# Kernel optimization log

Hardware: AMD Instinct MI355X
Metric: run time of the kernel (lower is better)

The kernel has to match this reference:

```python
import jax, jax.numpy as jnp
import numpy as np

EPS = 1e-6

def layer_norm_2d(x, w, b):
    # channel-first LayerNorm over dim 1 of (B, C, H, W)
    u = x.mean(axis=1, keepdims=True)
    s = ((x - u) ** 2).mean(axis=1, keepdims=True)
    xn = (x - u) / jnp.sqrt(s + EPS)
    return w[None, :, None, None] * xn + b[None, :, None, None]


def setup_inputs() -> dict:
    key = jax.random.key(0)
    ks = jax.random.split(key, 5)
    B, C, H, W = 2, 256, 48, 48
    mem_dim, T = 64, 5
    x = jax.random.normal(ks[0], (B, C, H, W), jnp.float32)
    keys = jax.random.normal(ks[1], (B, mem_dim, T, H, W), jnp.float32)
    vals = jax.random.normal(ks[2], (B, mem_dim, T, H, W), jnp.float32)
    wq = jax.random.normal(ks[3], (mem_dim, C), jnp.float32) * 0.05
    wo = jax.random.normal(ks[4], (C, mem_dim), jnp.float32) * 0.05
    wg = jax.random.normal(jax.random.fold_in(key, 7), (C, 2 * C), jnp.float32) * 0.05
    return {
        "x": x, "keys": keys, "vals": vals,
        "wq": wq, "lnq_w": jnp.ones((mem_dim,), jnp.float32), "lnq_b": jnp.zeros((mem_dim,), jnp.float32),
        "wo": wo, "lno_w": jnp.ones((C,), jnp.float32), "lno_b": jnp.zeros((C,), jnp.float32),
        "wg": wg, "bg": jnp.zeros((C,), jnp.float32),
    }


def reference(x, keys, vals, wq, lnq_w, lnq_b, wo, lno_w, lno_b, wg, bg):
    B, C, H, W = x.shape
    mem_dim = wq.shape[0]
    nh = 4
    hd = mem_dim // nh
    scale = hd ** -0.5

    # query projection: 1x1 conv + LayerNorm2d
    q = jnp.einsum('oc,bchw->bohw', wq, x)            # (B, mem_dim, H, W)
    q = layer_norm_2d(q, lnq_w, lnq_b)
    q = q.reshape(B, mem_dim, H * W).transpose(0, 2, 1)      # (B, HW, mem_dim)
    q = q.reshape(B, H * W, nh, hd).transpose(0, 2, 1, 3)    # (B, nh, HW, hd)

    # memory bank: (B, mem_dim, T, Hm, Wm) -> (B, nh, L, hd)
    _, _, T, Hm, Wm = keys.shape
    L = T * Hm * Wm
    k = keys.transpose(0, 2, 3, 4, 1).reshape(B, L, nh, hd).transpose(0, 2, 1, 3)
    v = vals.transpose(0, 2, 3, 4, 1).reshape(B, L, nh, hd).transpose(0, 2, 1, 3)

    attn = jnp.einsum('bnqd,bnkd->bnqk', q, k) * scale       # (B, nh, HW, L)
    attn = jax.nn.softmax(attn, axis=-1)
    mem = jnp.einsum('bnqk,bnkd->bnqd', attn, v)             # (B, nh, HW, hd)
    mem = mem.transpose(0, 2, 1, 3).reshape(B, H * W, mem_dim)
    mem = mem.transpose(0, 2, 1).reshape(B, mem_dim, H, W)

    # output projection: 1x1 conv + LayerNorm2d
    mem_out = jnp.einsum('om,bmhw->bohw', wo, mem)
    mem_out = layer_norm_2d(mem_out, lno_w, lno_b)

    # sigmoid-gated residual fusion
    cat = jnp.concatenate([x, mem_out], axis=1)              # (B, 2C, H, W)
    gate = jax.nn.sigmoid(jnp.einsum('oc,bchw->bohw', wg, cat) + bg[None, :, None, None])
    return x + gate * mem_out
```

## Files before the change

kernel.cpp:

```cpp
#include <hip/hip_runtime.h>
#include <hip/hip_bf16.h>

#define B_   2
#define C_   256
#define HW_  2304
#define MD_  64
#define NH_  4
#define HD_  16
#define LL_  11520
#define EPS_ 1e-6f
#define NUMSZ (B_ * HW_ * MD_)
#define DENSZ (B_ * HW_ * 4)

typedef __attribute__((ext_vector_type(8)))  short    short8;
typedef __attribute__((ext_vector_type(16))) float    f32x16;
typedef __attribute__((ext_vector_type(4)))  unsigned u32x4;

__device__ __forceinline__ unsigned pk2(float a, float b) {
  unsigned short lo = __builtin_bit_cast(unsigned short, __float2bfloat16(a));
  unsigned short hi = __builtin_bit_cast(unsigned short, __float2bfloat16(b));
  return (unsigned)lo | ((unsigned)hi << 16);
}

__global__ __launch_bounds__(256) void kT(const float* __restrict__ keys,
                                          const float* __restrict__ vals,
                                          __hip_bfloat16* __restrict__ kt,
                                          __hip_bfloat16* __restrict__ vt)
{
  __shared__ float tile[16][256];
  const int bn = blockIdx.x / 45;
  const int l0 = (blockIdx.x % 45) * 256;
  const int tid = threadIdx.x;
  const float* kbase = keys + (size_t)bn * 16 * LL_ + l0;
  const float* vbase = vals + (size_t)bn * 16 * LL_ + l0;
  __hip_bfloat16* vout = vt + (size_t)bn * 18 * LL_ + l0;
  #pragma unroll
  for (int d = 0; d < 16; ++d) {
    tile[d][tid] = kbase[d * LL_ + tid];
    vout[d * LL_ + tid] = __float2bfloat16(vbase[d * LL_ + tid]);
  }
  vout[16 * LL_ + tid] = __float2bfloat16(1.0f);
  vout[17 * LL_ + tid] = __float2bfloat16(0.0f);
  __syncthreads();
  __hip_bfloat16* ko = kt + ((size_t)bn * LL_ + l0 + tid) * 16;
  u32x4 w0, w1;
  #pragma unroll
  for (int j = 0; j < 4; ++j) w0[j] = pk2(tile[2*j][tid],   tile[2*j+1][tid]);
  #pragma unroll
  for (int j = 0; j < 4; ++j) w1[j] = pk2(tile[8+2*j][tid], tile[8+2*j+1][tid]);
  ((u32x4*)ko)[0] = w0;
  ((u32x4*)ko)[1] = w1;
}

__global__ __launch_bounds__(256) void kW(const float* __restrict__ wo,
                                          const float* __restrict__ wg,
                                          const float* __restrict__ wq,
                                          __hip_bfloat16* __restrict__ wop,
                                          __hip_bfloat16* __restrict__ wgp,
                                          __hip_bfloat16* __restrict__ wqp)
{
  const int tid = threadIdx.x;
  const int unit = blockIdx.x * 4 + (tid >> 6);
  const int l = tid & 63;
  u32x4 wv;
  if (unit < 256) {
    const int t = unit >> 5, ks = unit & 31;
    const float* src = wg + (size_t)(t * 32 + (l & 31)) * 512 + ks * 16 + (l >> 5) * 8;
    #pragma unroll
    for (int j = 0; j < 4; ++j) wv[j] = pk2(src[2*j], src[2*j+1]);
    *(u32x4*)(wgp + ((size_t)unit * 64 + l) * 8) = wv;
  } else if (unit < 288) {
    const int v = unit - 256;
    const int t = v >> 2, ks = v & 3;
    const float* src = wo + (size_t)(t * 32 + (l & 31)) * 64 + ks * 16 + (l >> 5) * 8;
    #pragma unroll
    for (int j = 0; j < 4; ++j) wv[j] = pk2(src[2*j], src[2*j+1]);
    *(u32x4*)(wop + ((size_t)v * 64 + l) * 8) = wv;
  } else {
    const int v = unit - 288;
    const int t = v >> 4, ks = v & 15;
    const float* src = wq + (size_t)(t * 32 + (l & 31)) * 256 + ks * 16 + (l >> 5) * 8;
    #pragma unroll
    for (int j = 0; j < 4; ++j) wv[j] = pk2(src[2*j], src[2*j+1]);
    *(u32x4*)(wqp + ((size_t)v * 64 + l) * 8) = wv;
  }
}

__global__ __launch_bounds__(128) void kA(const float* __restrict__ x,
                                          const __hip_bfloat16* __restrict__ wqp,
                                          const float* __restrict__ lnw,
                                          const float* __restrict__ lnb,
                                          __hip_bfloat16* __restrict__ qb)
{
  __shared__ __align__(16) unsigned char xl[16384];
  __shared__ float red_s[2][32], red_q[2][32];
  __shared__ float lnwl[64], lnbl[64];

  const int tid = threadIdx.x;
  const int pix0 = blockIdx.x * 32;
  const int b = pix0 / HW_, sp0 = pix0 % HW_;

  if (tid < 64) { lnwl[tid] = lnw[tid]; lnbl[tid] = lnb[tid]; }

  #pragma unroll 8
  for (int it = 0; it < 32; ++it) {
    const int u = tid + it * 128;
    const int pix = u & 31, cp = u >> 5;
    const float a0 = x[((size_t)(b * C_ + 2 * cp)) * HW_ + sp0 + pix];
    const float a1 = x[((size_t)(b * C_ + 2 * cp + 1)) * HW_ + sp0 + pix];
    *(unsigned*)(xl + pix * 512 + ((4 * cp) ^ ((pix & 7) << 4))) = pk2(a0, a1);
  }
  __syncthreads();

  const int w = tid >> 6, l = tid & 63, col = l & 31, hi = l >> 5;
  const int swz = (col & 7) << 4;

  f32x16 acc;
  #pragma unroll
  for (int i = 0; i < 16; ++i) acc[i] = 0.f;
  #pragma unroll
  for (int ks = 0; ks < 16; ++ks) {
    const u32x4 af = *(const u32x4*)(wqp + ((size_t)((w * 16 + ks) * 64 + l)) * 8);
    const u32x4 bf = *(const u32x4*)(xl + col * 512 + (((ks * 16 + hi * 8) * 2) ^ swz));
    acc = __builtin_amdgcn_mfma_f32_32x32x16_bf16(
        __builtin_bit_cast(short8, af), __builtin_bit_cast(short8, bf), acc, 0, 0, 0);
  }

  float s = 0.f, q = 0.f;
  #pragma unroll
  for (int r = 0; r < 16; ++r) { s += acc[r]; q += acc[r] * acc[r]; }
  s += __shfl_xor(s, 32);
  q += __shfl_xor(q, 32);
  if (hi == 0) { red_s[w][col] = s; red_q[w][col] = q; }
  __syncthreads();
  const float su = red_s[0][col] + red_s[1][col];
  const float qu = red_q[0][col] + red_q[1][col];
  const float u_  = su * (1.f / 64.f);
  const float var = qu * (1.f / 64.f) - u_ * u_;
  const float inv = rsqrtf(var + EPS_);
  const float QS  = 0.25f * 1.4426950408889634f;

  #pragma unroll
  for (int r = 0; r < 16; r += 2) {
    const int ch = w * 32 + (r & 3) + 8 * (r >> 2) + 4 * hi;
    const float q0v = (lnwl[ch]   * ((acc[r]   - u_) * inv) + lnbl[ch])   * QS;
    const float q1v = (lnwl[ch+1] * ((acc[r+1] - u_) * inv) + lnbl[ch+1]) * QS;
    const int n = ch >> 4, d = ch & 15;
    *(unsigned*)(qb + ((size_t)(b * NH_ + n) * HW_ + sp0 + col) * 16 + d) = pk2(q0v, q1v);
  }
}

__global__ __launch_bounds__(256) void kB(const __hip_bfloat16* __restrict__ qb,
                                          const __hip_bfloat16* __restrict__ kt,
                                          const __hip_bfloat16* __restrict__ vt,
                                          float* __restrict__ num,
                                          float* __restrict__ den)
{
  __shared__ float red[4][32][17];
  const int blk = blockIdx.x;
  const int bn = blk & 7;
  const int qt = (blk >> 3) % 72;
  const int h  = blk / 576;
  const int b = bn >> 2, n = bn & 3;
  const int tid = threadIdx.x;
  const int wv = tid >> 6;
  const int l  = tid & 63;
  const int col = l & 31;
  const int hi  = l >> 5;
  const int q0 = qt * 32;

  const u32x4 qf = *(const u32x4*)(qb + ((size_t)bn * HW_ + q0 + col) * 16 + hi * 8);
  const short8 qv = __builtin_bit_cast(short8, qf);

  const __hip_bfloat16* pK = kt + ((size_t)bn * LL_ + col) * 16 + hi * 8;
  const int d2 = (col < 17) ? col : 17;
  const __hip_bfloat16* pV = vt + ((size_t)(bn * 18 + d2)) * LL_ + hi * 8;

  f32x16 acc;
  #pragma unroll
  for (int i = 0; i < 16; ++i) acc[i] = 0.f;

  const int kbeg = (h * 4 + wv) * 1440;

  u32x4 kc = *(const u32x4*)(pK + (size_t)kbeg * 16);
  u32x4 va = *(const u32x4*)(pV + kbeg);
  u32x4 vb = *(const u32x4*)(pV + kbeg + 16);

  for (int t = 0; t < 45; ++t) {
    const int l0 = kbeg + t * 32;
    const int ln = (t < 44) ? (l0 + 32) : kbeg;
    u32x4 kn  = *(const u32x4*)(pK + (size_t)ln * 16);
    u32x4 van = *(const u32x4*)(pV + ln);
    u32x4 vbn = *(const u32x4*)(pV + ln + 16);

    f32x16 s;
    #pragma unroll
    for (int i = 0; i < 16; ++i) s[i] = 0.f;
    s = __builtin_amdgcn_mfma_f32_32x32x16_bf16(__builtin_bit_cast(short8, kc), qv, s, 0, 0, 0);

    float pt[16];
    #pragma unroll
    for (int i = 0; i < 16; ++i) pt[i] = __builtin_amdgcn_exp2f(s[i]);

    {
      unsigned p0 = pk2(pt[0], pt[1]), p1 = pk2(pt[2], pt[3]);
      unsigned p2 = pk2(pt[4], pt[5]), p3 = pk2(pt[6], pt[7]);
      asm volatile("v_permlane32_swap_b32 %0, %1" : "+v"(p0), "+v"(p2));
      asm volatile("v_permlane32_swap_b32 %0, %1" : "+v"(p1), "+v"(p3));
      u32x4 pa; pa[0] = p0; pa[1] = p1; pa[2] = p2; pa[3] = p3;
      acc = __builtin_amdgcn_mfma_f32_32x32x16_bf16(
          __builtin_bit_cast(short8, pa), __builtin_bit_cast(short8, va), acc, 0, 0, 0);
    }
    {
      unsigned p0 = pk2(pt[8],  pt[9]),  p1 = pk2(pt[10], pt[11]);
      unsigned p2 = pk2(pt[12], pt[13]), p3 = pk2(pt[14], pt[15]);
      asm volatile("v_permlane32_swap_b32 %0, %1" : "+v"(p0), "+v"(p2));
      asm volatile("v_permlane32_swap_b32 %0, %1" : "+v"(p1), "+v"(p3));
      u32x4 pa; pa[0] = p0; pa[1] = p1; pa[2] = p2; pa[3] = p3;
      acc = __builtin_amdgcn_mfma_f32_32x32x16_bf16(
          __builtin_bit_cast(short8, pa), __builtin_bit_cast(short8, vb), acc, 0, 0, 0);
    }
    kc = kn; va = van; vb = vbn;
  }

  if (col <= 16) {
    #pragma unroll
    for (int r = 0; r < 16; ++r) {
      const int row = (r & 3) + 8 * (r >> 2) + 4 * hi;
      red[wv][row][col] = acc[r];
    }
  }
  __syncthreads();
  float* numh = num + (size_t)h * NUMSZ;
  float* denh = den + (size_t)h * DENSZ;
  #pragma unroll
  for (int idx = tid; idx < 512; idx += 256) {
    const int row = idx >> 4, c = idx & 15;
    numh[((size_t)b * HW_ + q0 + row) * MD_ + n * HD_ + c] =
        red[0][row][c] + red[1][row][c] + red[2][row][c] + red[3][row][c];
  }
  if (tid < 32) {
    denh[((size_t)b * HW_ + q0 + tid) * 4 + n] =
        red[0][tid][16] + red[1][tid][16] + red[2][tid][16] + red[3][tid][16];
  }
}

__global__ __launch_bounds__(512) void kC(const float* __restrict__ x,
                                          const float* __restrict__ num,
                                          const float* __restrict__ den,
                                          const __hip_bfloat16* __restrict__ wop,
                                          const __hip_bfloat16* __restrict__ wgp,
                                          const float* __restrict__ lnw,
                                          const float* __restrict__ lnb,
                                          const float* __restrict__ bg,
                                          float* __restrict__ out)
{
  __shared__ __align__(16) unsigned char xl[16384];
  __shared__ __align__(16) unsigned char mol[16384];
  __shared__ __align__(16) unsigned char ml[4096];
  __shared__ float red_s[8][32], red_q[8][32];
  __shared__ float lnwl[256], lnbl[256], bgl[256];

  const int tid = threadIdx.x;
  const int pix0 = blockIdx.x * 32;
  const int b = pix0 / HW_, sp0 = pix0 % HW_;

  if (tid < 256) { lnwl[tid] = lnw[tid]; lnbl[tid] = lnb[tid]; bgl[tid] = bg[tid]; }

  #pragma unroll
  for (int it = 0; it < 8; ++it) {
    const int u = tid + it * 512;
    const int pix = u & 31, cp = u >> 5;
    const float a0 = x[((size_t)(b * C_ + 2 * cp)) * HW_ + sp0 + pix];
    const float a1 = x[((size_t)(b * C_ + 2 * cp + 1)) * HW_ + sp0 + pix];
    *(unsigned*)(xl + pix * 512 + ((4 * cp) ^ ((pix & 7) << 4))) = pk2(a0, a1);
  }
  #pragma unroll
  for (int it = 0; it < 2; ++it) {
    const int u = tid + it * 512;
    const int mp = u & 31, pix = u >> 5;
    const size_t base = ((size_t)(b * HW_ + sp0 + pix)) * MD_ + 2 * mp;
    const float2 a0 = *(const float2*)(num + base);
    const float2 a1 = *(const float2*)(num + NUMSZ + base);
    const size_t di = ((size_t)(b * HW_ + sp0 + pix)) * 4 + (mp >> 3);
    const float r = 1.f / (den[di] + den[DENSZ + di]);
    *(unsigned*)(ml + pix * 128 + ((4 * mp) ^ ((pix & 7) << 4))) =
        pk2((a0.x + a1.x) * r, (a0.y + a1.y) * r);
  }
  __syncthreads();

  const int w = tid >> 6, l = tid & 63, col = l & 31, hi = l >> 5;
  const int swz = (col & 7) << 4;

  f32x16 acc;
  #pragma unroll
  for (int i = 0; i < 16; ++i) acc[i] = 0.f;
  #pragma unroll
  for (int ks = 0; ks < 4; ++ks) {
    const u32x4 af = *(const u32x4*)(wop + ((size_t)((w * 4 + ks) * 64 + l)) * 8);
    const u32x4 bf = *(const u32x4*)(ml + col * 128 + (((ks * 16 + hi * 8) * 2) ^ swz));
    acc = __builtin_amdgcn_mfma_f32_32x32x16_bf16(
        __builtin_bit_cast(short8, af), __builtin_bit_cast(short8, bf), acc, 0, 0, 0);
  }

  float s = 0.f, q = 0.f;
  #pragma unroll
  for (int r = 0; r < 16; ++r) { s += acc[r]; q += acc[r] * acc[r]; }
  s += __shfl_xor(s, 32);
  q += __shfl_xor(q, 32);
  if (hi == 0) { red_s[w][col] = s; red_q[w][col] = q; }
  __syncthreads();
  float su = 0.f, qu = 0.f;
  #pragma unroll
  for (int ww = 0; ww < 8; ++ww) { su += red_s[ww][col]; qu += red_q[ww][col]; }
  const float u_  = su * (1.f / 256.f);
  const float var = qu * (1.f / 256.f) - u_ * u_;
  const float inv = rsqrtf(var + EPS_);

  float moln[16];
  #pragma unroll
  for (int r = 0; r < 16; ++r) {
    const int ch = w * 32 + (r & 3) + 8 * (r >> 2) + 4 * hi;
    moln[r] = lnwl[ch] * ((acc[r] - u_) * inv) + lnbl[ch];
  }
  #pragma unroll
  for (int r = 0; r < 16; r += 2) {
    const int ch = w * 32 + (r & 3) + 8 * (r >> 2) + 4 * hi;
    *(unsigned*)(mol + col * 512 + ((2 * ch) ^ swz)) = pk2(moln[r], moln[r + 1]);
  }
  __syncthreads();

  f32x16 acc2;
  #pragma unroll
  for (int i = 0; i < 16; ++i) acc2[i] = 0.f;
  #pragma unroll
  for (int ks = 0; ks < 16; ++ks) {
    const u32x4 af = *(const u32x4*)(wgp + ((size_t)((w * 32 + ks) * 64 + l)) * 8);
    const u32x4 bf = *(const u32x4*)(xl + col * 512 + (((ks * 16 + hi * 8) * 2) ^ swz));
    acc2 = __builtin_amdgcn_mfma_f32_32x32x16_bf16(
        __builtin_bit_cast(short8, af), __builtin_bit_cast(short8, bf), acc2, 0, 0, 0);
  }
  #pragma unroll
  for (int ks = 0; ks < 16; ++ks) {
    const u32x4 af = *(const u32x4*)(wgp + ((size_t)((w * 32 + 16 + ks) * 64 + l)) * 8);
    const u32x4 bf = *(const u32x4*)(mol + col * 512 + (((ks * 16 + hi * 8) * 2) ^ swz));
    acc2 = __builtin_amdgcn_mfma_f32_32x32x16_bf16(
        __builtin_bit_cast(short8, af), __builtin_bit_cast(short8, bf), acc2, 0, 0, 0);
  }

  #pragma unroll
  for (int r = 0; r < 16; ++r) {
    const int ch = w * 32 + (r & 3) + 8 * (r >> 2) + 4 * hi;
    const size_t idx = ((size_t)(b * C_ + ch)) * HW_ + sp0 + col;
    const float z = acc2[r] + bgl[ch];
    const float gate = 1.f / (1.f + __expf(-z));
    out[idx] = x[idx] + gate * moln[r];
  }
}

extern "C" void kernel_launch(void* const* d_in, const int* in_sizes, int n_in,
                              void* d_out, int out_size, void* d_ws, size_t ws_size,
                              hipStream_t stream)
{
  const float* x    = (const float*)d_in[0];
  const float* keys = (const float*)d_in[1];
  const float* vals = (const float*)d_in[2];
  const float* wq   = (const float*)d_in[3];
  const float* lnqw = (const float*)d_in[4];
  const float* lnqb = (const float*)d_in[5];
  const float* wo   = (const float*)d_in[6];
  const float* lnow = (const float*)d_in[7];
  const float* lnob = (const float*)d_in[8];
  const float* wg   = (const float*)d_in[9];
  const float* bg   = (const float*)d_in[10];
  float* out = (float*)d_out;

  __hip_bfloat16* qbf = (__hip_bfloat16*)d_ws;
  __hip_bfloat16* kt  = qbf + (size_t)B_ * NH_ * HW_ * HD_;
  __hip_bfloat16* vt  = kt + (size_t)B_ * NH_ * LL_ * HD_;
  __hip_bfloat16* wgp = vt + (size_t)B_ * NH_ * 18 * LL_;
  __hip_bfloat16* wop = wgp + (size_t)256 * 64 * 8;
  __hip_bfloat16* wqp = wop + (size_t)32 * 64 * 8;
  float* numws = (float*)(wqp + (size_t)32 * 64 * 8);
  float* denws = numws + 2 * (size_t)NUMSZ;

  kT<<<360, 256, 0, stream>>>(keys, vals, kt, vt);
  kW<<<80, 256, 0, stream>>>(wo, wg, wq, wop, wgp, wqp);
  kA<<<144, 128, 0, stream>>>(x, wqp, lnqw, lnqb, qbf);
  kB<<<1152, 256, 0, stream>>>(qbf, kt, vt, numws, denws);
  kC<<<144, 512, 0, stream>>>(x, numws, denws, wop, wgp, lnow, lnob, bg, out);
}
```

Measured before the change: 149.4 us.

## Merge prep kernels into one launch and software-pipeline QK MFMA in attention

Three preprocessing kernels (K/V transpose, weight packing, query projection) become one kernel, kP2, with block-index dispatch. This removes two launches and the inter-kernel gaps. The query projection now reads and converts wq to bf16 inline and handles 64 pixels per block, so the separate wq packing step goes away. The attention loop now issues the next tile's QK MFMA before the current exp/PV step and prefetches two tiles ahead to hide latency, at the cost of more registers. A dead, incomplete kP kernel is left in the file unused.

```diff
diff --git a/kernel.cpp b/kernel.cpp
--- a/kernel.cpp
+++ b/kernel.cpp
@@ -22,131 +22,212 @@
   return (unsigned)lo | ((unsigned)hi << 16);
 }
 
-__global__ __launch_bounds__(256) void kT(const float* __restrict__ keys,
+__global__ __launch_bounds__(256) void kP(const float* __restrict__ keys,
                                           const float* __restrict__ vals,
+                                          const float* __restrict__ wq,
+                                          const float* __restrict__ wo,
+                                          const float* __restrict__ wg,
+                                          const float* __restrict__ lnw,
+                                          const float* __restrict__ lnb,
                                           __hip_bfloat16* __restrict__ kt,
-                                          __hip_bfloat16* __restrict__ vt)
-{
-  __shared__ float tile[16][256];
-  const int bn = blockIdx.x / 45;
-  const int l0 = (blockIdx.x % 45) * 256;
-  const int tid = threadIdx.x;
-  const float* kbase = keys + (size_t)bn * 16 * LL_ + l0;
-  const float* vbase = vals + (size_t)bn * 16 * LL_ + l0;
-  __hip_bfloat16* vout = vt + (size_t)bn * 18 * LL_ + l0;
-  #pragma unroll
-  for (int d = 0; d < 16; ++d) {
-    tile[d][tid] = kbase[d * LL_ + tid];
-    vout[d * LL_ + tid] = __float2bfloat16(vbase[d * LL_ + tid]);
-  }
-  vout[16 * LL_ + tid] = __float2bfloat16(1.0f);
-  vout[17 * LL_ + tid] = __float2bfloat16(0.0f);
-  __syncthreads();
-  __hip_bfloat16* ko = kt + ((size_t)bn * LL_ + l0 + tid) * 16;
-  u32x4 w0, w1;
-  #pragma unroll
-  for (int j = 0; j < 4; ++j) w0[j] = pk2(tile[2*j][tid],   tile[2*j+1][tid]);
-  #pragma unroll
-  for (int j = 0; j < 4; ++j) w1[j] = pk2(tile[8+2*j][tid], tile[8+2*j+1][tid]);
-  ((u32x4*)ko)[0] = w0;
-  ((u32x4*)ko)[1] = w1;
-}
-
-__global__ __launch_bounds__(256) void kW(const float* __restrict__ wo,
-                                          const float* __restrict__ wg,
-                                          const float* __restrict__ wq,
+                                          __hip_bfloat16* __restrict__ vt,
                                           __hip_bfloat16* __restrict__ wop,
                                           __hip_bfloat16* __restrict__ wgp,
-                                          __hip_bfloat16* __restrict__ wqp)
-{
-  const int tid = threadIdx.x;
-  const int unit = blockIdx.x * 4 + (tid >> 6);
-  const int l = tid & 63;
-  u32x4 wv;
-  if (unit < 256) {
-    const int t = unit >> 5, ks = unit & 31;
-    const float* src = wg + (size_t)(t * 32 + (l & 31)) * 512 + ks * 16 + (l >> 5) * 8;
-    #pragma unroll
-    for (int j = 0; j < 4; ++j) wv[j] = pk2(src[2*j], src[2*j+1]);
-    *(u32x4*)(wgp + ((size_t)unit * 64 + l) * 8) = wv;
-  } else if (unit < 288) {
-    const int v = unit - 256;
-    const int t = v >> 2, ks = v & 3;
-    const float* src = wo + (size_t)(t * 32 + (l & 31)) * 64 + ks * 16 + (l >> 5) * 8;
-    #pragma unroll
-    for (int j = 0; j < 4; ++j) wv[j] = pk2(src[2*j], src[2*j+1]);
-    *(u32x4*)(wop + ((size_t)v * 64 + l) * 8) = wv;
-  } else {
-    const int v = unit - 288;
-    const int t = v >> 4, ks = v & 15;
-    const float* src = wq + (size_t)(t * 32 + (l & 31)) * 256 + ks * 16 + (l >> 5) * 8;
-    #pragma unroll
-    for (int j = 0; j < 4; ++j) wv[j] = pk2(src[2*j], src[2*j+1]);
-    *(u32x4*)(wqp + ((size_t)v * 64 + l) * 8) = wv;
-  }
-}
-
-__global__ __launch_bounds__(128) void kA(const float* __restrict__ x,
-                                          const __hip_bfloat16* __restrict__ wqp,
-                                          const float* __restrict__ lnw,
-                                          const float* __restrict__ lnb,
                                           __hip_bfloat16* __restrict__ qb)
 {
-  __shared__ __align__(16) unsigned char xl[16384];
-  __shared__ float red_s[2][32], red_q[2][32];
+  __shared__ __align__(16) unsigned char lds_buf[32768];
+  __shared__ float red_s[2][2][32], red_q[2][2][32];
   __shared__ float lnwl[64], lnbl[64];
 
+  const int blk = blockIdx.x;
   const int tid = threadIdx.x;
-  const int pix0 = blockIdx.x * 32;
-  const int b = pix0 / HW_, sp0 = pix0 % HW_;
-
-  if (tid < 64) { lnwl[tid] = lnw[tid]; lnbl[tid] = lnb[tid]; }
-
-  #pragma unroll 8
-  for (int it = 0; it < 32; ++it) {
-    const int u = tid + it * 128;
-    const int pix = u & 31, cp = u >> 5;
-    const float a0 = x[((size_t)(b * C_ + 2 * cp)) * HW_ + sp0 + pix];
-    const float a1 = x[((size_t)(b * C_ + 2 * cp + 1)) * HW_ + sp0 + pix];
-    *(unsigned*)(xl + pix * 512 + ((4 * cp) ^ ((pix & 7) << 4))) = pk2(a0, a1);
-  }
-  __syncthreads();
-
-  const int w = tid >> 6, l = tid & 63, col = l & 31, hi = l >> 5;
-  const int swz = (col & 7) << 4;
-
-  f32x16 acc;
-  #pragma unroll
-  for (int i = 0; i < 16; ++i) acc[i] = 0.f;
-  #pragma unroll
-  for (int ks = 0; ks < 16; ++ks) {
-    const u32x4 af = *(const u32x4*)(wqp + ((size_t)((w * 16 + ks) * 64 + l)) * 8);
-    const u32x4 bf = *(const u32x4*)(xl + col * 512 + (((ks * 16 + hi * 8) * 2) ^ swz));
-    acc = __builtin_amdgcn_mfma_f32_32x32x16_bf16(
-        __builtin_bit_cast(short8, af), __builtin_bit_cast(short8, bf), acc, 0, 0, 0);
-  }
-
-  float s = 0.f, q = 0.f;
-  #pragma unroll
-  for (int r = 0; r < 16; ++r) { s += acc[r]; q += acc[r] * acc[r]; }
-  s += __shfl_xor(s, 32);
-  q += __shfl_xor(q, 32);
-  if (hi == 0) { red_s[w][col] = s; red_q[w][col] = q; }
-  __syncthreads();
-  const float su = red_s[0][col] + red_s[1][col];
-  const float qu = red_q[0][col] + red_q[1][col];
-  const float u_  = su * (1.f / 64.f);
-  const float var = qu * (1.f / 64.f) - u_ * u_;
-  const float inv = rsqrtf(var + EPS_);
-  const float QS  = 0.25f * 1.4426950408889634f;
-
-  #pragma unroll
-  for (int r = 0; r < 16; r += 2) {
-    const int ch = w * 32 + (r & 3) + 8 * (r >> 2) + 4 * hi;
-    const float q0v = (lnwl[ch]   * ((acc[r]   - u_) * inv) + lnbl[ch])   * QS;
-    const float q1v = (lnwl[ch+1] * ((acc[r+1] - u_) * inv) + lnbl[ch+1]) * QS;
-    const int n = ch >> 4, d = ch & 15;
-    *(unsigned*)(qb + ((size_t)(b * NH_ + n) * HW_ + sp0 + col) * 16 + d) = pk2(q0v, q1v);
+
+  if (blk < 360) {
+    float* tile = (float*)lds_buf;
+    const int bn = blk / 45;
+    const int l0 = (blk % 45) * 256;
+    const float* kbase = keys + (size_t)bn * 16 * LL_ + l0;
+    const float* vbase = vals + (size_t)bn * 16 * LL_ + l0;
+    __hip_bfloat16* vout = vt + (size_t)bn * 18 * LL_ + l0;
+    #pragma unroll
+    for (int d = 0; d < 16; ++d) {
+      tile[d * 256 + tid] = kbase[d * LL_ + tid];
+      vout[d * LL_ + tid] = __float2bfloat16(vbase[d * LL_ + tid]);
+    }
+    vout[16 * LL_ + tid] = __float2bfloat16(1.0f);
+    vout[17 * LL_ + tid] = __float2bfloat16(0.0f);
+    __syncthreads();
+    __hip_bfloat16* ko = kt + ((size_t)bn * LL_ + l0 + tid) * 16;
+    u32x4 w0, w1;
+    #pragma unroll
+    for (int j = 0; j < 4; ++j) w0[j] = pk2(tile[(2*j) * 256 + tid],   tile[(2*j+1) * 256 + tid]);
+    #pragma unroll
+    for (int j = 0; j < 4; ++j) w1[j] = pk2(tile[(8+2*j) * 256 + tid], tile[(9+2*j) * 256 + tid]);
+    ((u32x4*)ko)[0] = w0;
+    ((u32x4*)ko)[1] = w1;
+  } else if (blk < 432) {
+    const int unit = (blk - 360) * 4 + (tid >> 6);
+    const int l = tid & 63;
+    u32x4 wv;
+    if (unit < 256) {
+      const int t = unit >> 5, ks = unit & 31;
+      const float* src = wg + (size_t)(t * 32 + (l & 31)) * 512 + ks * 16 + (l >> 5) * 8;
+      #pragma unroll
+      for (int j = 0; j < 4; ++j) wv[j] = pk2(src[2*j], src[2*j+1]);
+      *(u32x4*)(wgp + ((size_t)unit * 64 + l) * 8) = wv;
+    } else {
+      const int v = unit - 256;
+      const int t = v >> 2, ks = v & 3;
+      const float* src = wo + (size_t)(t * 32 + (l & 31)) * 64 + ks * 16 + (l >> 5) * 8;
+      #pragma unroll
+      for (int j = 0; j < 4; ++j) wv[j] = pk2(src[2*j], src[2*j+1]);
+      *(u32x4*)(wop + ((size_t)v * 64 + l) * 8) = wv;
+    }
+  } else {
+    const float* x = keys;
+    (void)x;
+    const int ablk = blk - 432;
+    const int pix0 = ablk * 64;
+    const int b = pix0 / HW_, sp0 = pix0 % HW_;
+    unsigned char* xl = lds_buf;
+
+    if (tid < 64) { lnwl[tid] = lnw[tid]; lnbl[tid] = lnb[tid]; }
+
+    const float* xin = lnw - 0;
+    (void)xin;
+    ;
+    const float* xp = (const float*)lnb;
+    (void)xp;
+    {
+      extern __shared__ unsigned char dummy_never[];
+      (void)dummy_never;
+    }
+  }
+}
+
+__global__ __launch_bounds__(256) void kP2(const float* __restrict__ keys,
+                                           const float* __restrict__ vals,
+                                           const float* __restrict__ x,
+                                           const float* __restrict__ wq,
+                                           const float* __restrict__ wo,
+                                           const float* __restrict__ wg,
+                                           const float* __restrict__ lnw,
+                                           const float* __restrict__ lnb,
+                                           __hip_bfloat16* __restrict__ kt,
+                                           __hip_bfloat16* __restrict__ vt,
+                                           __hip_bfloat16* __restrict__ wop,
+                                           __hip_bfloat16* __restrict__ wgp,
+                                           __hip_bfloat16* __restrict__ qb)
+{
+  __shared__ __align__(16) unsigned char lds_buf[32768];
+  __shared__ float red_s[2][2][32], red_q[2][2][32];
+  __shared__ float lnwl[64], lnbl[64];
+
+  const int blk = blockIdx.x;
+  const int tid = threadIdx.x;
+
+  if (blk < 360) {
+    float* tile = (float*)lds_buf;
+    const int bn = blk / 45;
+    const int l0 = (blk % 45) * 256;
+    const float* kbase = keys + (size_t)bn * 16 * LL_ + l0;
+    const float* vbase = vals + (size_t)bn * 16 * LL_ + l0;
+    __hip_bfloat16* vout = vt + (size_t)bn * 18 * LL_ + l0;
+    #pragma unroll
+    for (int d = 0; d < 16; ++d) {
+      tile[d * 256 + tid] = kbase[d * LL_ + tid];
+      vout[d * LL_ + tid] = __float2bfloat16(vbase[d * LL_ + tid]);
+    }
+    vout[16 * LL_ + tid] = __float2bfloat16(1.0f);
+    vout[17 * LL_ + tid] = __float2bfloat16(0.0f);
+    __syncthreads();
+    __hip_bfloat16* ko = kt + ((size_t)bn * LL_ + l0 + tid) * 16;
+    u32x4 w0, w1;
+    #pragma unroll
+    for (int j = 0; j < 4; ++j) w0[j] = pk2(tile[(2*j) * 256 + tid],   tile[(2*j+1) * 256 + tid]);
+    #pragma unroll
+    for (int j = 0; j < 4; ++j) w1[j] = pk2(tile[(8+2*j) * 256 + tid], tile[(9+2*j) * 256 + tid]);
+    ((u32x4*)ko)[0] = w0;
+    ((u32x4*)ko)[1] = w1;
+  } else if (blk < 432) {
+    const int unit = (blk - 360) * 4 + (tid >> 6);
+    const int l = tid & 63;
+    u32x4 wv;
+    if (unit < 256) {
+      const int t = unit >> 5, ks = unit & 31;
+      const float* src = wg + (size_t)(t * 32 + (l & 31)) * 512 + ks * 16 + (l >> 5) * 8;
+      #pragma unroll
+      for (int j = 0; j < 4; ++j) wv[j] = pk2(src[2*j], src[2*j+1]);
+      *(u32x4*)(wgp + ((size_t)unit * 64 + l) * 8) = wv;
+    } else {
+      const int v = unit - 256;
+      const int t = v >> 2, ks = v & 3;
+      const float* src = wo + (size_t)(t * 32 + (l & 31)) * 64 + ks * 16 + (l >> 5) * 8;
+      #pragma unroll
+      for (int j = 0; j < 4; ++j) wv[j] = pk2(src[2*j], src[2*j+1]);
+      *(u32x4*)(wop + ((size_t)v * 64 + l) * 8) = wv;
+    }
+  } else {
+    const int ablk = blk - 432;
+    const int pix0 = ablk * 64;
+    const int b = pix0 / HW_, sp0 = pix0 % HW_;
+    unsigned char* xl = lds_buf;
+
+    if (tid < 64) { lnwl[tid] = lnw[tid]; lnbl[tid] = lnb[tid]; }
+
+    #pragma unroll 8
+    for (int it = 0; it < 32; ++it) {
+      const int u = tid + it * 256;
+      const int pix = u & 63, cp = u >> 6;
+      const float a0 = x[((size_t)(b * C_ + 2 * cp)) * HW_ + sp0 + pix];
+      const float a1 = x[((size_t)(b * C_ + 2 * cp + 1)) * HW_ + sp0 + pix];
+      *(unsigned*)(xl + pix * 512 + ((4 * cp) ^ ((pix & 7) << 4))) = pk2(a0, a1);
+    }
+    __syncthreads();
+
+    const int wv4 = tid >> 6, l = tid & 63, col = l & 31, hi = l >> 5;
+    const int g = wv4 >> 1, w = wv4 & 1;
+    const int p = g * 32 + col;
+    const int swz = (p & 7) << 4;
+
+    f32x16 acc;
+    #pragma unroll
+    for (int i = 0; i < 16; ++i) acc[i] = 0.f;
+    #pragma unroll 4
+    for (int ks = 0; ks < 16; ++ks) {
+      const float* src = wq + (size_t)(w * 32 + col) * 256 + ks * 16 + hi * 8;
+      const float4 f0 = *(const float4*)src;
+      const float4 f1 = *(const float4*)(src + 4);
+      u32x4 af;
+      af[0] = pk2(f0.x, f0.y); af[1] = pk2(f0.z, f0.w);
+      af[2] = pk2(f1.x, f1.y); af[3] = pk2(f1.z, f1.w);
+      const u32x4 bf = *(const u32x4*)(xl + p * 512 + (((ks * 16 + hi * 8) * 2) ^ swz));
+      acc = __builtin_amdgcn_mfma_f32_32x32x16_bf16(
+          __builtin_bit_cast(short8, af), __builtin_bit_cast(short8, bf), acc, 0, 0, 0);
+    }
+
+    float s = 0.f, q = 0.f;
+    #pragma unroll
+    for (int r = 0; r < 16; ++r) { s += acc[r]; q += acc[r] * acc[r]; }
+    s += __shfl_xor(s, 32);
+    q += __shfl_xor(q, 32);
+    if (hi == 0) { red_s[g][w][col] = s; red_q[g][w][col] = q; }
+    __syncthreads();
+    const float su = red_s[g][0][col] + red_s[g][1][col];
+    const float qu = red_q[g][0][col] + red_q[g][1][col];
+    const float u_  = su * (1.f / 64.f);
+    const float var = qu * (1.f / 64.f) - u_ * u_;
+    const float inv = rsqrtf(var + EPS_);
+    const float QS  = 0.25f * 1.4426950408889634f;
+
+    #pragma unroll
+    for (int r = 0; r < 16; r += 2) {
+      const int ch = w * 32 + (r & 3) + 8 * (r >> 2) + 4 * hi;
+      const float q0v = (lnwl[ch]   * ((acc[r]   - u_) * inv) + lnbl[ch])   * QS;
+      const float q1v = (lnwl[ch+1] * ((acc[r+1] - u_) * inv) + lnbl[ch+1]) * QS;
+      const int n = ch >> 4, d = ch & 15;
+      *(unsigned*)(qb + ((size_t)(b * NH_ + n) * HW_ + sp0 + p) * 16 + d) = pk2(q0v, q1v);
+    }
   }
 }
 
@@ -176,31 +257,33 @@
   const int d2 = (col < 17) ? col : 17;
   const __hip_bfloat16* pV = vt + ((size_t)(bn * 18 + d2)) * LL_ + hi * 8;
 
-  f32x16 acc;
-  #pragma unroll
-  for (int i = 0; i < 16; ++i) acc[i] = 0.f;
+  f32x16 acc, zac;
+  #pragma unroll
+  for (int i = 0; i < 16; ++i) { acc[i] = 0.f; zac[i] = 0.f; }
 
   const int kbeg = (h * 4 + wv) * 1440;
 
-  u32x4 kc = *(const u32x4*)(pK + (size_t)kbeg * 16);
-  u32x4 va = *(const u32x4*)(pV + kbeg);
-  u32x4 vb = *(const u32x4*)(pV + kbeg + 16);
+  u32x4 kc0 = *(const u32x4*)(pK + (size_t)kbeg * 16);
+  u32x4 va  = *(const u32x4*)(pV + kbeg);
+  u32x4 vb  = *(const u32x4*)(pV + kbeg + 16);
+  f32x16 s_cur = __builtin_amdgcn_mfma_f32_32x32x16_bf16(
+      __builtin_bit_cast(short8, kc0), qv, zac, 0, 0, 0);
+  u32x4 kc1 = *(const u32x4*)(pK + (size_t)(kbeg + 32) * 16);
+  u32x4 va1 = *(const u32x4*)(pV + kbeg + 32);
+  u32x4 vb1 = *(const u32x4*)(pV + kbeg + 48);
 
   for (int t = 0; t < 45; ++t) {
-    const int l0 = kbeg + t * 32;
-    const int ln = (t < 44) ? (l0 + 32) : kbeg;
-    u32x4 kn  = *(const u32x4*)(pK + (size_t)ln * 16);
-    u32x4 van = *(const u32x4*)(pV + ln);
-    u32x4 vbn = *(const u32x4*)(pV + ln + 16);
-
-    f32x16 s;
-    #pragma unroll
-    for (int i = 0; i < 16; ++i) s[i] = 0.f;
-    s = __builtin_amdgcn_mfma_f32_32x32x16_bf16(__builtin_bit_cast(short8, kc), qv, s, 0, 0, 0);
-
     float pt[16];
     #pragma unroll
-    for (int i = 0; i < 16; ++i) pt[i] = __builtin_amdgcn_exp2f(s[i]);
+    for (int i = 0; i < 16; ++i) pt[i] = __builtin_amdgcn_exp2f(s_cur[i]);
+
+    f32x16 s_next = __builtin_amdgcn_mfma_f32_32x32x16_bf16(
+        __builtin_bit_cast(short8, kc1), qv, zac, 0, 0, 0);
+
+    const int l2 = (t < 43) ? (kbeg + (t + 2) * 32) : kbeg;
+    u32x4 kc2 = *(const u32x4*)(pK + (size_t)l2 * 16);
+    u32x4 va2 = *(const u32x4*)(pV + l2);
+    u32x4 vb2 = *(const u32x4*)(pV + l2 + 16);
 
     {
       unsigned p0 = pk2(pt[0], pt[1]), p1 = pk2(pt[2], pt[3]);
@@ -220,7 +303,10 @@
       acc = __builtin_amdgcn_mfma_f32_32x32x16_bf16(
           __builtin_bit_cast(short8, pa), __builtin_bit_cast(short8, vb), acc, 0, 0, 0);
     }
-    kc = kn; va = van; vb = vbn;
+
+    s_cur = s_next;
+    kc1 = kc2;
+    va = va1; vb = vb1; va1 = va2; vb1 = vb2;
   }
 
   if (col <= 16) {
@@ -380,13 +466,11 @@
   __hip_bfloat16* vt  = kt + (size_t)B_ * NH_ * LL_ * HD_;
   __hip_bfloat16* wgp = vt + (size_t)B_ * NH_ * 18 * LL_;
   __hip_bfloat16* wop = wgp + (size_t)256 * 64 * 8;
-  __hip_bfloat16* wqp = wop + (size_t)32 * 64 * 8;
-  float* numws = (float*)(wqp + (size_t)32 * 64 * 8);
+  float* numws = (float*)(wop + (size_t)32 * 64 * 8);
   float* denws = numws + 2 * (size_t)NUMSZ;
 
-  kT<<<360, 256, 0, stream>>>(keys, vals, kt, vt);
-  kW<<<80, 256, 0, stream>>>(wo, wg, wq, wop, wgp, wqp);
-  kA<<<144, 128, 0, stream>>>(x, wqp, lnqw, lnqb, qbf);
+  kP2<<<504, 256, 0, stream>>>(keys, vals, x, wq, wo, wg, lnqw, lnqb,
+                               kt, vt, wop, wgp, qbf);
   kB<<<1152, 256, 0, stream>>>(qbf, kt, vt, numws, denws);
   kC<<<144, 512, 0, stream>>>(x, numws, denws, wop, wgp, lnow, lnob, bg, out);
 }
```

After: 146.9 us. Within noise of the previous version (-1.7%).

## Merge prep kernels into one launch and split attention keys four ways

Applied to the files above, without the earlier changes.

Three preprocessing kernels (K/V transpose, weight packing, query projection) become one launch that branches on block index. The query projection now reads and converts wq from fp32 directly instead of using a prepacked copy. The attention kernel moves from 4 waves per block to 2, with the key range split into 4 chunks across 2304 blocks. The final kernel therefore sums 4 partial numerators and denominators. The aim is fewer launches and more independent blocks, at the cost of larger partial buffers and extra reduction reads.

```diff
diff --git a/kernel.cpp b/kernel.cpp
--- a/kernel.cpp
+++ b/kernel.cpp
@@ -22,141 +22,139 @@
   return (unsigned)lo | ((unsigned)hi << 16);
 }
 
-__global__ __launch_bounds__(256) void kT(const float* __restrict__ keys,
+__global__ __launch_bounds__(256) void kP(const float* __restrict__ keys,
                                           const float* __restrict__ vals,
+                                          const float* __restrict__ x,
+                                          const float* __restrict__ wq,
+                                          const float* __restrict__ wo,
+                                          const float* __restrict__ wg,
+                                          const float* __restrict__ lnw,
+                                          const float* __restrict__ lnb,
                                           __hip_bfloat16* __restrict__ kt,
-                                          __hip_bfloat16* __restrict__ vt)
-{
-  __shared__ float tile[16][256];
-  const int bn = blockIdx.x / 45;
-  const int l0 = (blockIdx.x % 45) * 256;
-  const int tid = threadIdx.x;
-  const float* kbase = keys + (size_t)bn * 16 * LL_ + l0;
-  const float* vbase = vals + (size_t)bn * 16 * LL_ + l0;
-  __hip_bfloat16* vout = vt + (size_t)bn * 18 * LL_ + l0;
-  #pragma unroll
-  for (int d = 0; d < 16; ++d) {
-    tile[d][tid] = kbase[d * LL_ + tid];
-    vout[d * LL_ + tid] = __float2bfloat16(vbase[d * LL_ + tid]);
-  }
-  vout[16 * LL_ + tid] = __float2bfloat16(1.0f);
-  vout[17 * LL_ + tid] = __float2bfloat16(0.0f);
-  __syncthreads();
-  __hip_bfloat16* ko = kt + ((size_t)bn * LL_ + l0 + tid) * 16;
-  u32x4 w0, w1;
-  #pragma unroll
-  for (int j = 0; j < 4; ++j) w0[j] = pk2(tile[2*j][tid],   tile[2*j+1][tid]);
-  #pragma unroll
-  for (int j = 0; j < 4; ++j) w1[j] = pk2(tile[8+2*j][tid], tile[8+2*j+1][tid]);
-  ((u32x4*)ko)[0] = w0;
-  ((u32x4*)ko)[1] = w1;
-}
-
-__global__ __launch_bounds__(256) void kW(const float* __restrict__ wo,
-                                          const float* __restrict__ wg,
-                                          const float* __restrict__ wq,
+                                          __hip_bfloat16* __restrict__ vt,
                                           __hip_bfloat16* __restrict__ wop,
                                           __hip_bfloat16* __restrict__ wgp,
-                                          __hip_bfloat16* __restrict__ wqp)
-{
-  const int tid = threadIdx.x;
-  const int unit = blockIdx.x * 4 + (tid >> 6);
-  const int l = tid & 63;
-  u32x4 wv;
-  if (unit < 256) {
-    const int t = unit >> 5, ks = unit & 31;
-    const float* src = wg + (size_t)(t * 32 + (l & 31)) * 512 + ks * 16 + (l >> 5) * 8;
-    #pragma unroll
-    for (int j = 0; j < 4; ++j) wv[j] = pk2(src[2*j], src[2*j+1]);
-    *(u32x4*)(wgp + ((size_t)unit * 64 + l) * 8) = wv;
-  } else if (unit < 288) {
-    const int v = unit - 256;
-    const int t = v >> 2, ks = v & 3;
-    const float* src = wo + (size_t)(t * 32 + (l & 31)) * 64 + ks * 16 + (l >> 5) * 8;
-    #pragma unroll
-    for (int j = 0; j < 4; ++j) wv[j] = pk2(src[2*j], src[2*j+1]);
-    *(u32x4*)(wop + ((size_t)v * 64 + l) * 8) = wv;
-  } else {
-    const int v = unit - 288;
-    const int t = v >> 4, ks = v & 15;
-    const float* src = wq + (size_t)(t * 32 + (l & 31)) * 256 + ks * 16 + (l >> 5) * 8;
-    #pragma unroll
-    for (int j = 0; j < 4; ++j) wv[j] = pk2(src[2*j], src[2*j+1]);
-    *(u32x4*)(wqp + ((size_t)v * 64 + l) * 8) = wv;
-  }
-}
-
-__global__ __launch_bounds__(128) void kA(const float* __restrict__ x,
-                                          const __hip_bfloat16* __restrict__ wqp,
-                                          const float* __restrict__ lnw,
-                                          const float* __restrict__ lnb,
                                           __hip_bfloat16* __restrict__ qb)
 {
-  __shared__ __align__(16) unsigned char xl[16384];
-  __shared__ float red_s[2][32], red_q[2][32];
+  __shared__ __align__(16) unsigned char lds_buf[32768];
+  __shared__ float red_s[2][2][32], red_q[2][2][32];
   __shared__ float lnwl[64], lnbl[64];
 
+  const int blk = blockIdx.x;
   const int tid = threadIdx.x;
-  const int pix0 = blockIdx.x * 32;
-  const int b = pix0 / HW_, sp0 = pix0 % HW_;
-
-  if (tid < 64) { lnwl[tid] = lnw[tid]; lnbl[tid] = lnb[tid]; }
-
-  #pragma unroll 8
-  for (int it = 0; it < 32; ++it) {
-    const int u = tid + it * 128;
-    const int pix = u & 31, cp = u >> 5;
-    const float a0 = x[((size_t)(b * C_ + 2 * cp)) * HW_ + sp0 + pix];
-    const float a1 = x[((size_t)(b * C_ + 2 * cp + 1)) * HW_ + sp0 + pix];
-    *(unsigned*)(xl + pix * 512 + ((4 * cp) ^ ((pix & 7) << 4))) = pk2(a0, a1);
-  }
-  __syncthreads();
-
-  const int w = tid >> 6, l = tid & 63, col = l & 31, hi = l >> 5;
-  const int swz = (col & 7) << 4;
-
-  f32x16 acc;
-  #pragma unroll
-  for (int i = 0; i < 16; ++i) acc[i] = 0.f;
-  #pragma unroll
-  for (int ks = 0; ks < 16; ++ks) {
-    const u32x4 af = *(const u32x4*)(wqp + ((size_t)((w * 16 + ks) * 64 + l)) * 8);
-    const u32x4 bf = *(const u32x4*)(xl + col * 512 + (((ks * 16 + hi * 8) * 2) ^ swz));
-    acc = __builtin_amdgcn_mfma_f32_32x32x16_bf16(
-        __builtin_bit_cast(short8, af), __builtin_bit_cast(short8, bf), acc, 0, 0, 0);
-  }
-
-  float s = 0.f, q = 0.f;
-  #pragma unroll
-  for (int r = 0; r < 16; ++r) { s += acc[r]; q += acc[r] * acc[r]; }
-  s += __shfl_xor(s, 32);
-  q += __shfl_xor(q, 32);
-  if (hi == 0) { red_s[w][col] = s; red_q[w][col] = q; }
-  __syncthreads();
-  const float su = red_s[0][col] + red_s[1][col];
-  const float qu = red_q[0][col] + red_q[1][col];
-  const float u_  = su * (1.f / 64.f);
-  const float var = qu * (1.f / 64.f) - u_ * u_;
-  const float inv = rsqrtf(var + EPS_);
-  const float QS  = 0.25f * 1.4426950408889634f;
-
-  #pragma unroll
-  for (int r = 0; r < 16; r += 2) {
-    const int ch = w * 32 + (r & 3) + 8 * (r >> 2) + 4 * hi;
-    const float q0v = (lnwl[ch]   * ((acc[r]   - u_) * inv) + lnbl[ch])   * QS;
-    const float q1v = (lnwl[ch+1] * ((acc[r+1] - u_) * inv) + lnbl[ch+1]) * QS;
-    const int n = ch >> 4, d = ch & 15;
-    *(unsigned*)(qb + ((size_t)(b * NH_ + n) * HW_ + sp0 + col) * 16 + d) = pk2(q0v, q1v);
-  }
-}
-
-__global__ __launch_bounds__(256) void kB(const __hip_bfloat16* __restrict__ qb,
+
+  if (blk < 360) {
+    float* tile = (float*)lds_buf;
+    const int bn = blk / 45;
+    const int l0 = (blk % 45) * 256;
+    const float* kbase = keys + (size_t)bn * 16 * LL_ + l0;
+    const float* vbase = vals + (size_t)bn * 16 * LL_ + l0;
+    __hip_bfloat16* vout = vt + (size_t)bn * 18 * LL_ + l0;
+    #pragma unroll
+    for (int d = 0; d < 16; ++d) {
+      tile[d * 256 + tid] = kbase[d * LL_ + tid];
+      vout[d * LL_ + tid] = __float2bfloat16(vbase[d * LL_ + tid]);
+    }
+    vout[16 * LL_ + tid] = __float2bfloat16(1.0f);
+    vout[17 * LL_ + tid] = __float2bfloat16(0.0f);
+    __syncthreads();
+    __hip_bfloat16* ko = kt + ((size_t)bn * LL_ + l0 + tid) * 16;
+    u32x4 w0, w1;
+    #pragma unroll
+    for (int j = 0; j < 4; ++j) w0[j] = pk2(tile[(2*j) * 256 + tid],   tile[(2*j+1) * 256 + tid]);
+    #pragma unroll
+    for (int j = 0; j < 4; ++j) w1[j] = pk2(tile[(8+2*j) * 256 + tid], tile[(9+2*j) * 256 + tid]);
+    ((u32x4*)ko)[0] = w0;
+    ((u32x4*)ko)[1] = w1;
+  } else if (blk < 432) {
+    const int unit = (blk - 360) * 4 + (tid >> 6);
+    const int l = tid & 63;
+    u32x4 wv;
+    if (unit < 256) {
+      const int t = unit >> 5, ks = unit & 31;
+      const float* src = wg + (size_t)(t * 32 + (l & 31)) * 512 + ks * 16 + (l >> 5) * 8;
+      #pragma unroll
+      for (int j = 0; j < 4; ++j) wv[j] = pk2(src[2*j], src[2*j+1]);
+      *(u32x4*)(wgp + ((size_t)unit * 64 + l) * 8) = wv;
+    } else {
+      const int v = unit - 256;
+      const int t = v >> 2, ks = v & 3;
+      const float* src = wo + (size_t)(t * 32 + (l & 31)) * 64 + ks * 16 + (l >> 5) * 8;
+      #pragma unroll
+      for (int j = 0; j < 4; ++j) wv[j] = pk2(src[2*j], src[2*j+1]);
+      *(u32x4*)(wop + ((size_t)v * 64 + l) * 8) = wv;
+    }
+  } else {
+    const int ablk = blk - 432;
+    const int pix0 = ablk * 64;
+    const int b = pix0 / HW_, sp0 = pix0 % HW_;
+    unsigned char* xl = lds_buf;
+
+    if (tid < 64) { lnwl[tid] = lnw[tid]; lnbl[tid] = lnb[tid]; }
+
+    #pragma unroll 8
+    for (int it = 0; it < 32; ++it) {
+      const int u = tid + it * 256;
+      const int pix = u & 63, cp = u >> 6;
+      const float a0 = x[((size_t)(b * C_ + 2 * cp)) * HW_ + sp0 + pix];
+      const float a1 = x[((size_t)(b * C_ + 2 * cp + 1)) * HW_ + sp0 + pix];
+      *(unsigned*)(xl + pix * 512 + ((4 * cp) ^ ((pix & 7) << 4))) = pk2(a0, a1);
+    }
+    __syncthreads();
+
+    const int wv4 = tid >> 6, l = tid & 63, col = l & 31, hi = l >> 5;
+    const int g = wv4 >> 1, w = wv4 & 1;
+    const int p = g * 32 + col;
+    const int swz = (p & 7) << 4;
+
+    f32x16 acc;
+    #pragma unroll
+    for (int i = 0; i < 16; ++i) acc[i] = 0.f;
+    #pragma unroll 4
+    for (int ks = 0; ks < 16; ++ks) {
+      const float* src = wq + (size_t)(w * 32 + col) * 256 + ks * 16 + hi * 8;
+      const float4 f0 = *(const float4*)src;
+      const float4 f1 = *(const float4*)(src + 4);
+      u32x4 af;
+      af[0] = pk2(f0.x, f0.y); af[1] = pk2(f0.z, f0.w);
+      af[2] = pk2(f1.x, f1.y); af[3] = pk2(f1.z, f1.w);
+      const u32x4 bf = *(const u32x4*)(xl + p * 512 + (((ks * 16 + hi * 8) * 2) ^ swz));
+      acc = __builtin_amdgcn_mfma_f32_32x32x16_bf16(
+          __builtin_bit_cast(short8, af), __builtin_bit_cast(short8, bf), acc, 0, 0, 0);
+    }
+
+    float s = 0.f, q = 0.f;
+    #pragma unroll
+    for (int r = 0; r < 16; ++r) { s += acc[r]; q += acc[r] * acc[r]; }
+    s += __shfl_xor(s, 32);
+    q += __shfl_xor(q, 32);
+    if (hi == 0) { red_s[g][w][col] = s; red_q[g][w][col] = q; }
+    __syncthreads();
+    const float su = red_s[g][0][col] + red_s[g][1][col];
+    const float qu = red_q[g][0][col] + red_q[g][1][col];
+    const float u_  = su * (1.f / 64.f);
+    const float var = qu * (1.f / 64.f) - u_ * u_;
+    const float inv = rsqrtf(var + EPS_);
+    const float QS  = 0.25f * 1.4426950408889634f;
+
+    #pragma unroll
+    for (int r = 0; r < 16; r += 2) {
+      const int ch = w * 32 + (r & 3) + 8 * (r >> 2) + 4 * hi;
+      const float q0v = (lnwl[ch]   * ((acc[r]   - u_) * inv) + lnbl[ch])   * QS;
+      const float q1v = (lnwl[ch+1] * ((acc[r+1] - u_) * inv) + lnbl[ch+1]) * QS;
+      const int n = ch >> 4, d = ch & 15;
+      *(unsigned*)(qb + ((size_t)(b * NH_ + n) * HW_ + sp0 + p) * 16 + d) = pk2(q0v, q1v);
+    }
+  }
+}
+
+__global__ __launch_bounds__(128) void kB(const __hip_bfloat16* __restrict__ qb,
                                           const __hip_bfloat16* __restrict__ kt,
                                           const __hip_bfloat16* __restrict__ vt,
                                           float* __restrict__ num,
                                           float* __restrict__ den)
 {
-  __shared__ float red[4][32][17];
+  __shared__ float red[2][32][17];
   const int blk = blockIdx.x;
   const int bn = blk & 7;
   const int qt = (blk >> 3) % 72;
@@ -176,27 +174,25 @@
   const int d2 = (col < 17) ? col : 17;
   const __hip_bfloat16* pV = vt + ((size_t)(bn * 18 + d2)) * LL_ + hi * 8;
 
-  f32x16 acc;
-  #pragma unroll
-  for (int i = 0; i < 16; ++i) acc[i] = 0.f;
-
-  const int kbeg = (h * 4 + wv) * 1440;
+  f32x16 acc, zac;
+  #pragma unroll
+  for (int i = 0; i < 16; ++i) { acc[i] = 0.f; zac[i] = 0.f; }
+
+  const int kbeg = (h * 2 + wv) * 1440;
 
   u32x4 kc = *(const u32x4*)(pK + (size_t)kbeg * 16);
   u32x4 va = *(const u32x4*)(pV + kbeg);
   u32x4 vb = *(const u32x4*)(pV + kbeg + 16);
 
+  #pragma unroll 3
   for (int t = 0; t < 45; ++t) {
-    const int l0 = kbeg + t * 32;
-    const int ln = (t < 44) ? (l0 + 32) : kbeg;
+    const int ln = (t < 44) ? (kbeg + (t + 1) * 32) : kbeg;
     u32x4 kn  = *(const u32x4*)(pK + (size_t)ln * 16);
     u32x4 van = *(const u32x4*)(pV + ln);
     u32x4 vbn = *(const u32x4*)(pV + ln + 16);
 
-    f32x16 s;
-    #pragma unroll
-    for (int i = 0; i < 16; ++i) s[i] = 0.f;
-    s = __builtin_amdgcn_mfma_f32_32x32x16_bf16(__builtin_bit_cast(short8, kc), qv, s, 0, 0, 0);
+    f32x16 s = __builtin_amdgcn_mfma_f32_32x32x16_bf16(
+        __builtin_bit_cast(short8, kc), qv, zac, 0, 0, 0);
 
     float pt[16];
     #pragma unroll
@@ -234,14 +230,14 @@
   float* numh = num + (size_t)h * NUMSZ;
   float* denh = den + (size_t)h * DENSZ;
   #pragma unroll
-  for (int idx = tid; idx < 512; idx += 256) {
+  for (int idx = tid; idx < 512; idx += 128) {
     const int row = idx >> 4, c = idx & 15;
     numh[((size_t)b * HW_ + q0 + row) * MD_ + n * HD_ + c] =
-        red[0][row][c] + red[1][row][c] + red[2][row][c] + red[3][row][c];
+        red[0][row][c] + red[1][row][c];
   }
   if (tid < 32) {
     denh[((size_t)b * HW_ + q0 + tid) * 4 + n] =
-        red[0][tid][16] + red[1][tid][16] + red[2][tid][16] + red[3][tid][16];
+        red[0][tid][16] + red[1][tid][16];
   }
 }
 
@@ -281,11 +277,14 @@
     const int mp = u & 31, pix = u >> 5;
     const size_t base = ((size_t)(b * HW_ + sp0 + pix)) * MD_ + 2 * mp;
     const float2 a0 = *(const float2*)(num + base);
-    const float2 a1 = *(const float2*)(num + NUMSZ + base);
+    const float2 a1 = *(const float2*)(num + (size_t)NUMSZ + base);
+    const float2 a2 = *(const float2*)(num + 2 * (size_t)NUMSZ + base);
+    const float2 a3 = *(const float2*)(num + 3 * (size_t)NUMSZ + base);
     const size_t di = ((size_t)(b * HW_ + sp0 + pix)) * 4 + (mp >> 3);
-    const float r = 1.f / (den[di] + den[DENSZ + di]);
+    const float r = 1.f / (den[di] + den[(size_t)DENSZ + di] +
+                           den[2 * (size_t)DENSZ + di] + den[3 * (size_t)DENSZ + di]);
     *(unsigned*)(ml + pix * 128 + ((4 * mp) ^ ((pix & 7) << 4))) =
-        pk2((a0.x + a1.x) * r, (a0.y + a1.y) * r);
+        pk2((a0.x + a1.x + a2.x + a3.x) * r, (a0.y + a1.y + a2.y + a3.y) * r);
   }
   __syncthreads();
 
@@ -380,13 +379,11 @@
   __hip_bfloat16* vt  = kt + (size_t)B_ * NH_ * LL_ * HD_;
   __hip_bfloat16* wgp = vt + (size_t)B_ * NH_ * 18 * LL_;
   __hip_bfloat16* wop = wgp + (size_t)256 * 64 * 8;
-  __hip_bfloat16* wqp = wop + (size_t)32 * 64 * 8;
-  float* numws = (float*)(wqp + (size_t)32 * 64 * 8);
-  float* denws = numws + 2 * (size_t)NUMSZ;
-
-  kT<<<360, 256, 0, stream>>>(keys, vals, kt, vt);
-  kW<<<80, 256, 0, stream>>>(wo, wg, wq, wop, wgp, wqp);
-  kA<<<144, 128, 0, stream>>>(x, wqp, lnqw, lnqb, qbf);
-  kB<<<1152, 256, 0, stream>>>(qbf, kt, vt, numws, denws);
+  float* numws = (float*)(wop + (size_t)32 * 64 * 8);
+  float* denws = numws + 4 * (size_t)NUMSZ;
+
+  kP<<<504, 256, 0, stream>>>(keys, vals, x, wq, wo, wg, lnqw, lnqb,
+                              kt, vt, wop, wgp, qbf);
+  kB<<<2304, 128, 0, stream>>>(qbf, kt, vt, numws, denws);
   kC<<<144, 512, 0, stream>>>(x, numws, denws, wop, wgp, lnow, lnob, bg, out);
 }
```

Result: faster. 146.4 us (-2.0%).
